# Kernel optimization log

Hardware: AMD Instinct MI355X
Metric: run time of the kernel (lower is better)

Reference implementation:

```python
import jax, jax.numpy as jnp
import numpy as np

N_X = 250_000
N_SRC = 50_000
N_Y = 50_000
N_INT = 500_000
E_NODE = 1_000_000
E_DOM = 500_000
H = 128
BN_EPS = 1e-5


def setup_inputs() -> dict:
    key = jax.random.key(0)
    ks = jax.random.split(key, 10)
    x = jax.random.normal(ks[0], (N_X, H), dtype=jnp.float32)
    y = jax.random.normal(ks[1], (N_Y, H), dtype=jnp.float32)
    domain_indicator = jnp.sort(jax.random.randint(ks[2], (N_X,), 0, N_SRC))
    node_map_edge_index = jax.random.randint(ks[3], (2, E_NODE), 0, N_X)
    intersect_indicator = jnp.sort(jax.random.randint(ks[4], (E_NODE,), 0, N_INT))
    domain_map_edge_index = jax.random.randint(ks[5], (2, E_DOM), 0, N_SRC)  # both rows < 50000 == N_SRC == N_Y
    W_xsum = jax.random.normal(ks[6], (H, H), dtype=jnp.float32) / np.sqrt(H)
    W_xint = jax.random.normal(ks[7], (H, H), dtype=jnp.float32) / np.sqrt(H)
    W_y = jax.random.normal(ks[8], (H, H), dtype=jnp.float32) / np.sqrt(H)
    bn_w = jnp.ones((H,), dtype=jnp.float32)
    bn_b = jnp.zeros((H,), dtype=jnp.float32)
    return {"x": x, "y": y, "domain_indicator": domain_indicator,
            "node_map_edge_index": node_map_edge_index,
            "intersect_indicator": intersect_indicator,
            "domain_map_edge_index": domain_map_edge_index,
            "W_xsum": W_xsum, "W_xint": W_xint, "W_y": W_y,
            "bn_w": bn_w, "bn_b": bn_b}


def reference(x, y, domain_indicator, node_map_edge_index, intersect_indicator,
              domain_map_edge_index, W_xsum, W_xint, W_y, bn_w, bn_b):
    # scatter_sum(x, source.domain_indicator) -> [N_SRC, H], then Linear (no bias)
    x_sum = jax.ops.segment_sum(x, domain_indicator, num_segments=N_SRC) @ W_xsum.T
    # gather nodes along node_map edges, scatter_sum into intersections -> [N_INT, H]
    x_int = jax.ops.segment_sum(x[node_map_edge_index[0]], intersect_indicator,
                                num_segments=N_INT) @ W_xint.T
    # per domain-map-edge messages, [E_DOM, H]
    x_msg = x_sum[domain_map_edge_index[0]] + x_int
    y_msg = y[domain_map_edge_index[1]] @ W_y.T
    msg = x_msg + y_msg
    # BatchNorm1d (training mode: batch stats, biased variance) + ReLU
    mean = jnp.mean(msg, axis=0)
    var = jnp.var(msg, axis=0)
    msg = (msg - mean) * jax.lax.rsqrt(var + BN_EPS) * bn_w + bn_b
    msg = jax.nn.relu(msg)
    # reduce messages onto target domains -> [N_Y, H]
    return jax.ops.segment_sum(msg, domain_map_edge_index[1], num_segments=N_Y)
```

## Files before the change

### kernel.cpp

```cpp
#include <hip/hip_runtime.h>
#include <cstdint>

#define HH 128
#define SB 136
constexpr int cN_X   = 250000;
constexpr int cN_SRC = 50000;
constexpr int cN_Y   = 50000;
constexpr int cN_INT = 500000;
constexpr int cE_NODE = 1000000;
constexpr int cE_DOM  = 500000;

typedef __attribute__((ext_vector_type(8))) short bf16x8;
typedef __attribute__((ext_vector_type(4))) float f32x4;

__device__ __forceinline__ float bf2f(unsigned short s) {
  union { unsigned u; float f; } v; v.u = ((unsigned)s) << 16; return v.f;
}
__device__ __forceinline__ unsigned short f2bf(float f) {
  union { float f; unsigned u; } v; v.f = f;
  unsigned r = v.u + 0x7fffu + ((v.u >> 16) & 1u);
  return (unsigned short)(r >> 16);
}

__global__ __launch_bounds__(256) void k_setup(const float* __restrict__ w0,
                                               const float* __restrict__ w1,
                                               const float* __restrict__ w2,
                                               unsigned short* __restrict__ dst,
                                               const int* __restrict__ ii,
                                               int* __restrict__ bnd,
                                               float* __restrict__ xsum,
                                               int* __restrict__ cnt,
                                               float* __restrict__ part2) {
  int b = blockIdx.x, tid = threadIdx.x;
  if (b < 48) {
    int i = b * 256 + tid;
    int idx4 = i * 4;
    int mat = idx4 >> 14;
    int off = idx4 & 16383;
    const float* src = (mat == 0) ? w0 : (mat == 1) ? w1 : w2;
    float4 v = *(const float4*)(src + off);
    ushort4 u;
    u.x = f2bf(v.x); u.y = f2bf(v.y); u.z = f2bf(v.z); u.w = f2bf(v.w);
    *(ushort4*)(dst + (size_t)mat * 16384 + off) = u;
    return;
  }
  b -= 48;
  if (b < 6250) {
    ((float4*)xsum)[(size_t)b * 256 + tid] = make_float4(0.f, 0.f, 0.f, 0.f);
    return;
  }
  b -= 6250;
  if (b < 49) {
    int i = b * 256 + tid;
    if (i < 12500) ((int4*)cnt)[i] = make_int4(0, 0, 0, 0);
    return;
  }
  b -= 49;
  if (b < 16) {
    ((float4*)part2)[b * 256 + tid] = make_float4(0.f, 0.f, 0.f, 0.f);
    return;
  }
  b -= 16;
  {
    int j = b * 256 + tid;
    if (j > cE_NODE) return;
    if (j == cE_NODE) {
      int a = ii[cE_NODE - 1];
      for (int e = a + 1; e <= cN_INT; ++e) bnd[e] = cE_NODE;
      return;
    }
    int bb = ii[j];
    int a = (j == 0) ? -1 : ii[j - 1];
    for (int e = a + 1; e <= bb; ++e) bnd[e] = j;
  }
}

__device__ __forceinline__ void load_bfrags(const unsigned short* __restrict__ Wbf,
                                            int wv, int lane, bf16x8 bfrag[2][4]) {
  int cbase = wv * 32 + (lane & 15);
  int krow = (lane >> 4) * 8;
#pragma unroll
  for (int ct = 0; ct < 2; ct++)
#pragma unroll
    for (int kt = 0; kt < 4; kt++)
      bfrag[ct][kt] = *(const bf16x8*)(Wbf + (size_t)(cbase + ct * 16) * HH + kt * 32 + krow);
}

__global__ __launch_bounds__(256, 4) void k_gemmx_segsum(
    const float* __restrict__ A, const int* __restrict__ ind,
    const unsigned short* __restrict__ Wbf,
    unsigned short* __restrict__ outb, float* __restrict__ xsum,
    const int* __restrict__ dme1, int* __restrict__ cnt) {
  __shared__ unsigned short sA[64 * SB];
  __shared__ int sind[64];
  int tid = threadIdx.x, lane = tid & 63, wv = tid >> 6;
  {
    int e = blockIdx.x * 256 + tid;
    if (e < cE_DOM) atomicAdd(&cnt[dme1[e]], 1);
  }
  int row0 = blockIdx.x * 64;
  int rows = min(64, cN_X - row0);
  if (tid < 64 && tid < rows) sind[tid] = ind[row0 + tid];
  bf16x8 bfrag[2][4];
  load_bfrags(Wbf, wv, lane, bfrag);
#pragma unroll
  for (int it = 0; it < 4; it++) {
    int g = it * 2048 + tid * 8;
    int r = g >> 7, c = g & 127;
    bf16x8 v = {0, 0, 0, 0, 0, 0, 0, 0};
    if (r < rows) {
      float4 f0 = *(const float4*)(A + (size_t)(row0 + r) * HH + c);
      float4 f1 = *(const float4*)(A + (size_t)(row0 + r) * HH + c + 4);
      v[0] = (short)f2bf(f0.x); v[1] = (short)f2bf(f0.y);
      v[2] = (short)f2bf(f0.z); v[3] = (short)f2bf(f0.w);
      v[4] = (short)f2bf(f1.x); v[5] = (short)f2bf(f1.y);
      v[6] = (short)f2bf(f1.z); v[7] = (short)f2bf(f1.w);
    }
    *(bf16x8*)(&sA[r * SB + c]) = v;
  }
  __syncthreads();
  {
    int rbase = wv * 16;
    if (rbase < rows) {
      int nr = min(16, rows - rbase);
      int c0 = lane * 2;
      unsigned xv[16];
#pragma unroll
      for (int k = 0; k < 16; k++)
        xv[k] = (k < nr) ? *(const unsigned*)(&sA[(rbase + k) * SB + c0]) : 0u;
      float a0 = 0.f, a1 = 0.f;
      int cur = sind[rbase];
      bool inside = false;
#pragma unroll
      for (int k = 0; k < 16; k++) {
        if (k < nr) {
          int s = sind[rbase + k];
          if (s != cur) {
            if (inside) {
              xsum[(size_t)cur * HH + c0] = a0;
              xsum[(size_t)cur * HH + c0 + 1] = a1;
            } else {
              atomicAdd(&xsum[(size_t)cur * HH + c0], a0);
              atomicAdd(&xsum[(size_t)cur * HH + c0 + 1], a1);
            }
            cur = s; a0 = 0.f; a1 = 0.f; inside = true;
          }
          a0 += bf2f(xv[k] & 0xffff); a1 += bf2f(xv[k] >> 16);
        }
      }
      atomicAdd(&xsum[(size_t)cur * HH + c0], a0);
      atomicAdd(&xsum[(size_t)cur * HH + c0 + 1], a1);
    }
  }
  int m = lane & 15, q = lane >> 4;
  f32x4 acc[4][2];
#pragma unroll
  for (int rt = 0; rt < 4; rt++)
#pragma unroll
    for (int ct = 0; ct < 2; ct++) acc[rt][ct] = (f32x4){0.f, 0.f, 0.f, 0.f};
#pragma unroll
  for (int kt = 0; kt < 4; kt++) {
    int kof = kt * 32 + q * 8;
#pragma unroll
    for (int rt = 0; rt < 4; rt++) {
      bf16x8 af = *(const bf16x8*)(&sA[(rt * 16 + m) * SB + kof]);
      acc[rt][0] = __builtin_amdgcn_mfma_f32_16x16x32_bf16(af, bfrag[0][kt], acc[rt][0], 0, 0, 0);
      acc[rt][1] = __builtin_amdgcn_mfma_f32_16x16x32_bf16(af, bfrag[1][kt], acc[rt][1], 0, 0, 0);
    }
  }
  __syncthreads();
  unsigned short* sC = sA;
#pragma unroll
  for (int rt = 0; rt < 4; rt++)
#pragma unroll
    for (int ct = 0; ct < 2; ct++)
#pragma unroll
      for (int rg = 0; rg < 4; rg++) {
        int r = rt * 16 + q * 4 + rg;
        sC[r * HH + wv * 32 + ct * 16 + m] = f2bf(acc[rt][ct][rg]);
      }
  __syncthreads();
  for (int i = tid; i < rows * 16; i += 256) {
    int r = i >> 4, g = i & 15;
    ((uint4*)(outb + (size_t)(row0 + r) * HH))[g] = ((const uint4*)(sC + r * HH))[g];
  }
}

__global__ __launch_bounds__(256, 4) void k_gemm2(const float* __restrict__ Axs,
                                                  const float* __restrict__ Ay,
                                                  const unsigned short* __restrict__ Wbf,
                                                  unsigned short* __restrict__ xsl,
                                                  unsigned short* __restrict__ ylin) {
  __shared__ unsigned short sA[64 * SB];
  int tid = threadIdx.x, lane = tid & 63, wv = tid >> 6;
  const int nbm = (cN_SRC + 63) / 64;
  bool isY = blockIdx.x >= nbm;
  const float* A = isY ? Ay : Axs;
  const unsigned short* W = Wbf + (isY ? 16384 : 0);
  unsigned short* outb = isY ? ylin : xsl;
  int bb = isY ? blockIdx.x - nbm : blockIdx.x;
  int row0 = bb * 64;
  int rows = min(64, cN_SRC - row0);
  bf16x8 bfrag[2][4];
  load_bfrags(W, wv, lane, bfrag);
#pragma unroll
  for (int it = 0; it < 4; it++) {
    int g = it * 2048 + tid * 8;
    int r = g >> 7, c = g & 127;
    bf16x8 v = {0, 0, 0, 0, 0, 0, 0, 0};
    if (r < rows) {
      float4 f0 = *(const float4*)(A + (size_t)(row0 + r) * HH + c);
      float4 f1 = *(const float4*)(A + (size_t)(row0 + r) * HH + c + 4);
      v[0] = (short)f2bf(f0.x); v[1] = (short)f2bf(f0.y);
      v[2] = (short)f2bf(f0.z); v[3] = (short)f2bf(f0.w);
      v[4] = (short)f2bf(f1.x); v[5] = (short)f2bf(f1.y);
      v[6] = (short)f2bf(f1.z); v[7] = (short)f2bf(f1.w);
    }
    *(bf16x8*)(&sA[r * SB + c]) = v;
  }
  __syncthreads();
  int m = lane & 15, q = lane >> 4;
  f32x4 acc[4][2];
#pragma unroll
  for (int rt = 0; rt < 4; rt++)
#pragma unroll
    for (int ct = 0; ct < 2; ct++) acc[rt][ct] = (f32x4){0.f, 0.f, 0.f, 0.f};
#pragma unroll
  for (int kt = 0; kt < 4; kt++) {
    int kof = kt * 32 + q * 8;
#pragma unroll
    for (int rt = 0; rt < 4; rt++) {
      bf16x8 af = *(const bf16x8*)(&sA[(rt * 16 + m) * SB + kof]);
      acc[rt][0] = __builtin_amdgcn_mfma_f32_16x16x32_bf16(af, bfrag[0][kt], acc[rt][0], 0, 0, 0);
      acc[rt][1] = __builtin_amdgcn_mfma_f32_16x16x32_bf16(af, bfrag[1][kt], acc[rt][1], 0, 0, 0);
    }
  }
  __syncthreads();
  unsigned short* sC = sA;
#pragma unroll
  for (int rt = 0; rt < 4; rt++)
#pragma unroll
    for (int ct = 0; ct < 2; ct++)
#pragma unroll
      for (int rg = 0; rg < 4; rg++) {
        int r = rt * 16 + q * 4 + rg;
        sC[r * HH + wv * 32 + ct * 16 + m] = f2bf(acc[rt][ct][rg]);
      }
  __syncthreads();
  for (int i = tid; i < rows * 16; i += 256) {
    int r = i >> 4, g = i & 15;
    ((uint4*)(outb + (size_t)(row0 + r) * HH))[g] = ((const uint4*)(sC + r * HH))[g];
  }
}

__global__ __launch_bounds__(256) void k_scan1(const int* __restrict__ cnt,
                                               int* __restrict__ bsum, int* __restrict__ excl) {
  __shared__ int buf[256];
  int i = blockIdx.x * 256 + threadIdx.x;
  int v = (i < cN_SRC) ? cnt[i] : 0;
  buf[threadIdx.x] = v; __syncthreads();
  for (int d = 1; d < 256; d <<= 1) {
    int t = (threadIdx.x >= d) ? buf[threadIdx.x - d] : 0;
    __syncthreads();
    buf[threadIdx.x] += t;
    __syncthreads();
  }
  if (i < cN_SRC) excl[i] = buf[threadIdx.x] - v;
  if (threadIdx.x == 255) bsum[blockIdx.x] = buf[255];
}
__global__ __launch_bounds__(256) void k_scan23(const int* __restrict__ excl,
                                                const int* __restrict__ bsum,
                                                int* __restrict__ offs,
                                                int* __restrict__ cursor, int nb) {
  __shared__ int buf[256];
  __shared__ int ex[256];
  int tid = threadIdx.x;
  int v = (tid < nb) ? bsum[tid] : 0;
  buf[tid] = v; __syncthreads();
  for (int d = 1; d < 256; d <<= 1) {
    int t = (tid >= d) ? buf[tid - d] : 0;
    __syncthreads();
    buf[tid] += t;
    __syncthreads();
  }
  ex[tid] = buf[tid] - v;
  __syncthreads();
  int i = blockIdx.x * 256 + tid;
  if (i < cN_SRC) { int o = excl[i] + ex[i >> 8]; offs[i] = o; cursor[i] = o; }
  else if (i == cN_SRC) offs[cN_SRC] = cE_DOM;
}
__global__ void k_scatter(const int* __restrict__ dme0, const int* __restrict__ dme1,
                          const int* __restrict__ bnd, int* __restrict__ cursor,
                          int4* __restrict__ rec) {
  int e = blockIdx.x * blockDim.x + threadIdx.x;
  if (e < cE_DOM) {
    int t = dme1[e];
    int pos = atomicAdd(&cursor[t], 1);
    int j0 = bnd[e];
    rec[pos] = make_int4(dme0[e], t, j0, bnd[e + 1] - j0);
  }
}

#define EDGE_ISSUE(I, B)                                                     \
  do {                                                                       \
    int le_ = wv * 8 + (I);                                                  \
    int n_ = __builtin_amdgcn_readfirstlane(sR[le_].w);                      \
    _Pragma("unroll")                                                        \
    for (int k_ = 0; k_ < 4; k_++) {                                         \
      int r_ = (k_ < n_) ? __builtin_amdgcn_readlane(idxv[I], k_) : 0;       \
      ub[B][k_] = xwu[(size_t)r_ * 64 + lane];                               \
    }                                                                        \
  } while (0)

#define EDGE_CONSUME(I, B)                                                   \
  do {                                                                       \
    int le_ = wv * 8 + (I);                                                  \
    int j0_ = __builtin_amdgcn_readfirstlane(sR[le_].z);                     \
    int n_ = __builtin_amdgcn_readfirstlane(sR[le_].w);                      \
    float a0_ = 0.f, a1_ = 0.f;                                              \
    _Pragma("unroll")                                                        \
    for (int k_ = 0; k_ < 4; k_++) {                                         \
      unsigned uv_ = (k_ < n_) ? ub[B][k_] : 0u;                             \
      a0_ += bf2f(uv_ & 0xffff);                                             \
      a1_ += bf2f(uv_ >> 16);                                                \
    }                                                                        \
    if (n_ > 4) {                                                            \
      for (int k_ = 4; k_ < n_; k_++) {                                      \
        int r_ = (k_ < 64) ? __builtin_amdgcn_readlane(idxv[I], k_)          \
                           : nme0[j0_ + k_];                                 \
        unsigned uu_ = xwu[(size_t)r_ * 64 + lane];                          \
        a0_ += bf2f(uu_ & 0xffff);                                           \
        a1_ += bf2f(uu_ >> 16);                                              \
      }                                                                      \
    }                                                                        \
    float m0_ = a0_ + bf2f(xs[I] & 0xffff) + bf2f(yy[I] & 0xffff);           \
    float m1_ = a1_ + bf2f(xs[I] >> 16) + bf2f(yy[I] >> 16);                 \
    unsigned um_ = ((unsigned)f2bf(m1_) << 16) | (unsigned)f2bf(m0_);        \
    __builtin_nontemporal_store(um_, &msgu[(size_t)(e0 + le_) * 64 + lane]); \
    s0 += m0_; q0 += m0_ * m0_; s1 += m1_; q1 += m1_ * m1_;                  \
  } while (0)

#define SBAR __builtin_amdgcn_sched_barrier(0)

__global__ __launch_bounds__(256, 8) void k_edge2(
    const unsigned* __restrict__ xwu, const int* __restrict__ nme0,
    const unsigned* __restrict__ xslu, const unsigned* __restrict__ ylu,
    const int4* __restrict__ rec,
    unsigned* __restrict__ msgu, float* __restrict__ part2) {
  __shared__ int4 sR[32];
  __shared__ float sBN[1024];
  int tid = threadIdx.x, lane = tid & 63, wv = tid >> 6;
  int e0 = blockIdx.x * 32;
  if (tid < 32) sR[tid] = rec[e0 + tid];
  __syncthreads();

  unsigned xs[8], yy[8];
  int idxv[8];
#pragma unroll
  for (int i = 0; i < 8; i++) {
    int le = wv * 8 + i;
    int s  = __builtin_amdgcn_readfirstlane(sR[le].x);
    int t  = __builtin_amdgcn_readfirstlane(sR[le].y);
    int j0 = __builtin_amdgcn_readfirstlane(sR[le].z);
    int n  = __builtin_amdgcn_readfirstlane(sR[le].w);
    xs[i] = xslu[(size_t)s * 64 + lane];
    yy[i] = ylu[(size_t)t * 64 + lane];
    idxv[i] = (lane < n) ? nme0[j0 + lane] : 0;
  }
  SBAR;

  float s0 = 0.f, q0 = 0.f, s1 = 0.f, q1 = 0.f;
  unsigned ub[3][4];
  EDGE_ISSUE(0, 0); SBAR;
  EDGE_ISSUE(1, 1); SBAR;
  EDGE_ISSUE(2, 2); SBAR;
  EDGE_CONSUME(0, 0);
  EDGE_ISSUE(3, 0); SBAR;
  EDGE_CONSUME(1, 1);
  EDGE_ISSUE(4, 1); SBAR;
  EDGE_CONSUME(2, 2);
  EDGE_ISSUE(5, 2); SBAR;
  EDGE_CONSUME(3, 0);
  EDGE_ISSUE(6, 0); SBAR;
  EDGE_CONSUME(4, 1);
  EDGE_ISSUE(7, 1); SBAR;
  EDGE_CONSUME(5, 2);
  EDGE_CONSUME(6, 0);
  EDGE_CONSUME(7, 1);

  *(float4*)(&sBN[wv * 256 + lane * 4]) = make_float4(s0, q0, s1, q1);
  __syncthreads();
  float v = sBN[tid] + sBN[256 + tid] + sBN[512 + tid] + sBN[768 + tid];
  atomicAdd(&part2[((blockIdx.x & 63) << 8) + tid], v);
}

__global__ __launch_bounds__(256) void k_bnfinal(const float* __restrict__ part2,
                                                 const float* __restrict__ bnw,
                                                 const float* __restrict__ bnb,
                                                 float* __restrict__ ss) {
  __shared__ float L[256];
  float s = 0.f;
  for (int b = 0; b < 64; b++) s += part2[b * 256 + threadIdx.x];
  L[threadIdx.x] = s; __syncthreads();
  if (threadIdx.x < HH) {
    int c = threadIdx.x;
    float sum = L[2 * c], sq = L[2 * c + 1];
    float mean = sum / (float)cE_DOM;
    float var = sq / (float)cE_DOM - mean * mean;
    float sc = bnw[c] * rsqrtf(var + 1e-5f);
    float sh = bnb[c] - mean * sc;
    ss[2 * c] = sc; ss[2 * c + 1] = sh;
  }
}

__global__ __launch_bounds__(256, 8) void k_out2(const unsigned* __restrict__ msgu,
                                                 const int* __restrict__ offs,
                                                 const float* __restrict__ ss,
                                                 float* __restrict__ out) {
  int wv = threadIdx.x >> 6, lane = threadIdx.x & 63;
  int t = blockIdx.x * 4 + wv;
  if (t >= cN_Y) return;
  int c0 = lane * 2;
  float sc0 = ss[c0 * 2 + 0], sh0 = ss[c0 * 2 + 1];
  float sc1 = ss[c0 * 2 + 2], sh1 = ss[c0 * 2 + 3];
  int j0 = __builtin_amdgcn_readfirstlane(offs[t]);
  int j1 = __builtin_amdgcn_readfirstlane(offs[t + 1]);
  float a0 = 0.f, a1 = 0.f;
  int p = j0;
  for (; p + 8 <= j1; p += 8) {
    unsigned m[8];
#pragma unroll
    for (int k = 0; k < 8; k++) m[k] = msgu[(size_t)(p + k) * 64 + lane];
    __builtin_amdgcn_sched_barrier(0);
#pragma unroll
    for (int k = 0; k < 8; k++) {
      a0 += fmaxf(fmaf(bf2f(m[k] & 0xffff), sc0, sh0), 0.f);
      a1 += fmaxf(fmaf(bf2f(m[k] >> 16), sc1, sh1), 0.f);
    }
  }
  if (p + 4 <= j1) {
    unsigned m[4];
#pragma unroll
    for (int k = 0; k < 4; k++) m[k] = msgu[(size_t)(p + k) * 64 + lane];
    __builtin_amdgcn_sched_barrier(0);
#pragma unroll
    for (int k = 0; k < 4; k++) {
      a0 += fmaxf(fmaf(bf2f(m[k] & 0xffff), sc0, sh0), 0.f);
      a1 += fmaxf(fmaf(bf2f(m[k] >> 16), sc1, sh1), 0.f);
    }
    p += 4;
  }
  for (; p < j1; p++) {
    unsigned m = msgu[(size_t)p * 64 + lane];
    a0 += fmaxf(fmaf(bf2f(m & 0xffff), sc0, sh0), 0.f);
    a1 += fmaxf(fmaf(bf2f(m >> 16), sc1, sh1), 0.f);
  }
  *(float2*)(out + (size_t)t * HH + c0) = make_float2(a0, a1);
}

extern "C" void kernel_launch(void* const* d_in, const int* in_sizes, int n_in,
                              void* d_out, int out_size, void* d_ws, size_t ws_size,
                              hipStream_t stream) {
  const float* x     = (const float*)d_in[0];
  const float* y     = (const float*)d_in[1];
  const int* dom_ind = (const int*)d_in[2];
  const int* nme     = (const int*)d_in[3];
  const int* ii      = (const int*)d_in[4];
  const int* dme     = (const int*)d_in[5];
  const float* Wxsum = (const float*)d_in[6];
  const float* Wxint = (const float*)d_in[7];
  const float* Wy    = (const float*)d_in[8];
  const float* bnw   = (const float*)d_in[9];
  const float* bnb   = (const float*)d_in[10];
  float* out = (float*)d_out;

  char* ws = (char*)d_ws;
  size_t o = 0;
  auto alloc = [&](size_t bytes) -> void* {
    void* p = ws + o;
    o = (o + bytes + 255) & ~(size_t)255;
    return p;
  };
  float* xsum   = (float*)alloc((size_t)cN_SRC * HH * 4);
  unsigned short* xsl = (unsigned short*)alloc((size_t)cN_SRC * HH * 2);
  unsigned short* ylin = (unsigned short*)alloc((size_t)cN_Y * HH * 2);
  unsigned short* xw = (unsigned short*)alloc((size_t)cN_X * HH * 2);
  unsigned short* msg = (unsigned short*)alloc((size_t)cE_DOM * HH * 2);
  int* bnd      = (int*)alloc((size_t)(cN_INT + 1) * 4);
  int* cnt      = (int*)alloc((size_t)cN_SRC * 4);
  int* excl     = (int*)alloc((size_t)cN_SRC * 4);
  int* bsum     = (int*)alloc(256 * 4);
  int* offs     = (int*)alloc((size_t)(cN_SRC + 1) * 4);
  int* cursor   = (int*)alloc((size_t)cN_SRC * 4);
  int4* rec     = (int4*)alloc((size_t)cE_DOM * 16);
  float* part2  = (float*)alloc(64 * 256 * 4);
  float* ssbuf  = (float*)alloc(256 * 4);
  unsigned short* Wbf = (unsigned short*)alloc(3 * 16384 * 2);

  const int nb_scan = (cN_SRC + 255) / 256;
  k_setup<<<48 + 6250 + 49 + 16 + 3907, 256, 0, stream>>>(Wxsum, Wy, Wxint, Wbf,
                                                          ii, bnd, xsum, cnt, part2);
  k_gemmx_segsum<<<(cN_X + 63) / 64, 256, 0, stream>>>(x, dom_ind, Wbf + 32768, xw, xsum,
                                                       dme + cE_DOM, cnt);
  k_gemm2<<<2 * ((cN_SRC + 63) / 64), 256, 0, stream>>>(xsum, y, Wbf, xsl, ylin);
  k_scan1<<<nb_scan, 256, 0, stream>>>(cnt, bsum, excl);
  k_scan23<<<(cN_SRC + 1 + 255) / 256, 256, 0, stream>>>(excl, bsum, offs, cursor, nb_scan);
  k_scatter<<<(cE_DOM + 255) / 256, 256, 0, stream>>>(dme, dme + cE_DOM, bnd, cursor, rec);
  k_edge2<<<cE_DOM / 32, 256, 0, stream>>>((const unsigned*)xw, nme,
                                           (const unsigned*)xsl, (const unsigned*)ylin,
                                           rec, (unsigned*)msg, part2);
  k_bnfinal<<<1, 256, 0, stream>>>(part2, bnw, bnb, ssbuf);
  k_out2<<<(cN_Y + 3) / 4, 256, 0, stream>>>((const unsigned*)msg, offs, ssbuf, out);
}
```

Baseline: 425.7 us.

## Fold y GEMM into setup, merge scan/scatter into cooperative kernel

The y@W_y GEMM moves into the setup kernel, since it depends only on inputs, and runs alongside the zeroing and boundary work. The separate weight-to-bf16 conversion is dropped, with each GEMM converting its fp32 weights directly into fragments. The two scan kernels and the scatter kernel become one cooperative kernel that uses grid syncs. This removes several launches and serial dependencies, at the cost of redundant weight conversion per block and the overhead of cooperative grid sync.

Measured after the change: 687.1 us. 61.4% more time.

```diff
diff --git a/kernel.cpp b/kernel.cpp
--- a/kernel.cpp
+++ b/kernel.cpp
@@ -1,5 +1,8 @@
 #include <hip/hip_runtime.h>
+#include <hip/hip_cooperative_groups.h>
 #include <cstdint>
+
+namespace cg = cooperative_groups;
 
 #define HH 128
 #define SB 136
@@ -22,29 +25,101 @@
   return (unsigned short)(r >> 16);
 }
 
-__global__ __launch_bounds__(256) void k_setup(const float* __restrict__ w0,
-                                               const float* __restrict__ w1,
-                                               const float* __restrict__ w2,
-                                               unsigned short* __restrict__ dst,
+__device__ __forceinline__ void load_bfrags_f32(const float* __restrict__ Wf,
+                                                int wv, int lane, bf16x8 bfrag[2][4]) {
+  int cbase = wv * 32 + (lane & 15);
+  int krow = (lane >> 4) * 8;
+#pragma unroll
+  for (int ct = 0; ct < 2; ct++)
+#pragma unroll
+    for (int kt = 0; kt < 4; kt++) {
+      const float* p = Wf + (size_t)(cbase + ct * 16) * HH + kt * 32 + krow;
+      float4 f0 = *(const float4*)p;
+      float4 f1 = *(const float4*)(p + 4);
+      bf16x8 v;
+      v[0] = (short)f2bf(f0.x); v[1] = (short)f2bf(f0.y);
+      v[2] = (short)f2bf(f0.z); v[3] = (short)f2bf(f0.w);
+      v[4] = (short)f2bf(f1.x); v[5] = (short)f2bf(f1.y);
+      v[6] = (short)f2bf(f1.z); v[7] = (short)f2bf(f1.w);
+      bfrag[ct][kt] = v;
+    }
+}
+
+__device__ __forceinline__ void gemm_tile(const float* __restrict__ A,
+                                          const float* __restrict__ Wf,
+                                          unsigned short* __restrict__ outb,
+                                          int row0, int rows,
+                                          unsigned short* sA, int tid) {
+  int lane = tid & 63, wv = tid >> 6;
+  bf16x8 bfrag[2][4];
+  load_bfrags_f32(Wf, wv, lane, bfrag);
+#pragma unroll
+  for (int it = 0; it < 4; it++) {
+    int g = it * 2048 + tid * 8;
+    int r = g >> 7, c = g & 127;
+    bf16x8 v = {0, 0, 0, 0, 0, 0, 0, 0};
+    if (r < rows) {
+      float4 f0 = *(const float4*)(A + (size_t)(row0 + r) * HH + c);
+      float4 f1 = *(const float4*)(A + (size_t)(row0 + r) * HH + c + 4);
+      v[0] = (short)f2bf(f0.x); v[1] = (short)f2bf(f0.y);
+      v[2] = (short)f2bf(f0.z); v[3] = (short)f2bf(f0.w);
+      v[4] = (short)f2bf(f1.x); v[5] = (short)f2bf(f1.y);
+      v[6] = (short)f2bf(f1.z); v[7] = (short)f2bf(f1.w);
+    }
+    *(bf16x8*)(&sA[r * SB + c]) = v;
+  }
+  __syncthreads();
+  int m = lane & 15, q = lane >> 4;
+  f32x4 acc[4][2];
+#pragma unroll
+  for (int rt = 0; rt < 4; rt++)
+#pragma unroll
+    for (int ct = 0; ct < 2; ct++) acc[rt][ct] = (f32x4){0.f, 0.f, 0.f, 0.f};
+#pragma unroll
+  for (int kt = 0; kt < 4; kt++) {
+    int kof = kt * 32 + q * 8;
+#pragma unroll
+    for (int rt = 0; rt < 4; rt++) {
+      bf16x8 af = *(const bf16x8*)(&sA[(rt * 16 + m) * SB + kof]);
+      acc[rt][0] = __builtin_amdgcn_mfma_f32_16x16x32_bf16(af, bfrag[0][kt], acc[rt][0], 0, 0, 0);
+      acc[rt][1] = __builtin_amdgcn_mfma_f32_16x16x32_bf16(af, bfrag[1][kt], acc[rt][1], 0, 0, 0);
+    }
+  }
+  __syncthreads();
+  unsigned short* sC = sA;
+#pragma unroll
+  for (int rt = 0; rt < 4; rt++)
+#pragma unroll
+    for (int ct = 0; ct < 2; ct++)
+#pragma unroll
+      for (int rg = 0; rg < 4; rg++) {
+        int r = rt * 16 + q * 4 + rg;
+        sC[r * HH + wv * 32 + ct * 16 + m] = f2bf(acc[rt][ct][rg]);
+      }
+  __syncthreads();
+  for (int i = tid; i < rows * 16; i += 256) {
+    int r = i >> 4, g = i & 15;
+    ((uint4*)(outb + (size_t)(row0 + r) * HH))[g] = ((const uint4*)(sC + r * HH))[g];
+  }
+}
+
+__global__ __launch_bounds__(256) void k_setup(const float* __restrict__ y,
+                                               const float* __restrict__ Wy,
+                                               unsigned short* __restrict__ ylin,
                                                const int* __restrict__ ii,
                                                int* __restrict__ bnd,
                                                float* __restrict__ xsum,
                                                int* __restrict__ cnt,
                                                float* __restrict__ part2) {
+  __shared__ unsigned short sA[64 * SB];
   int b = blockIdx.x, tid = threadIdx.x;
-  if (b < 48) {
-    int i = b * 256 + tid;
-    int idx4 = i * 4;
-    int mat = idx4 >> 14;
-    int off = idx4 & 16383;
-    const float* src = (mat == 0) ? w0 : (mat == 1) ? w1 : w2;
-    float4 v = *(const float4*)(src + off);
-    ushort4 u;
-    u.x = f2bf(v.x); u.y = f2bf(v.y); u.z = f2bf(v.z); u.w = f2bf(v.w);
-    *(ushort4*)(dst + (size_t)mat * 16384 + off) = u;
+  if (b < 782) {
+    int row0 = b * 64;
+    int rows = min(64, cN_Y - row0);
+    gemm_tile(y, Wy, ylin, row0, rows, sA, tid);
     return;
   }
-  b -= 48;
+  b -= 782;
   if (b < 6250) {
     ((float4*)xsum)[(size_t)b * 256 + tid] = make_float4(0.f, 0.f, 0.f, 0.f);
     return;
@@ -75,20 +150,9 @@
   }
 }
 
-__device__ __forceinline__ void load_bfrags(const unsigned short* __restrict__ Wbf,
-                                            int wv, int lane, bf16x8 bfrag[2][4]) {
-  int cbase = wv * 32 + (lane & 15);
-  int krow = (lane >> 4) * 8;
-#pragma unroll
-  for (int ct = 0; ct < 2; ct++)
-#pragma unroll
-    for (int kt = 0; kt < 4; kt++)
-      bfrag[ct][kt] = *(const bf16x8*)(Wbf + (size_t)(cbase + ct * 16) * HH + kt * 32 + krow);
-}
-
 __global__ __launch_bounds__(256, 4) void k_gemmx_segsum(
     const float* __restrict__ A, const int* __restrict__ ind,
-    const unsigned short* __restrict__ Wbf,
+    const float* __restrict__ Wxint,
     unsigned short* __restrict__ outb, float* __restrict__ xsum,
     const int* __restrict__ dme1, int* __restrict__ cnt) {
   __shared__ unsigned short sA[64 * SB];
@@ -102,7 +166,7 @@
   int rows = min(64, cN_X - row0);
   if (tid < 64 && tid < rows) sind[tid] = ind[row0 + tid];
   bf16x8 bfrag[2][4];
-  load_bfrags(Wbf, wv, lane, bfrag);
+  load_bfrags_f32(Wxint, wv, lane, bfrag);
 #pragma unroll
   for (int it = 0; it < 4; it++) {
     int g = it * 2048 + tid * 8;
@@ -186,114 +250,60 @@
   }
 }
 
-__global__ __launch_bounds__(256, 4) void k_gemm2(const float* __restrict__ Axs,
-                                                  const float* __restrict__ Ay,
-                                                  const unsigned short* __restrict__ Wbf,
-                                                  unsigned short* __restrict__ xsl,
-                                                  unsigned short* __restrict__ ylin) {
+__global__ __launch_bounds__(256, 4) void k_gemmxsl(const float* __restrict__ xsum,
+                                                    const float* __restrict__ Wxsum,
+                                                    unsigned short* __restrict__ xsl) {
   __shared__ unsigned short sA[64 * SB];
-  int tid = threadIdx.x, lane = tid & 63, wv = tid >> 6;
-  const int nbm = (cN_SRC + 63) / 64;
-  bool isY = blockIdx.x >= nbm;
-  const float* A = isY ? Ay : Axs;
-  const unsigned short* W = Wbf + (isY ? 16384 : 0);
-  unsigned short* outb = isY ? ylin : xsl;
-  int bb = isY ? blockIdx.x - nbm : blockIdx.x;
-  int row0 = bb * 64;
+  int row0 = blockIdx.x * 64;
   int rows = min(64, cN_SRC - row0);
-  bf16x8 bfrag[2][4];
-  load_bfrags(W, wv, lane, bfrag);
-#pragma unroll
-  for (int it = 0; it < 4; it++) {
-    int g = it * 2048 + tid * 8;
-    int r = g >> 7, c = g & 127;
-    bf16x8 v = {0, 0, 0, 0, 0, 0, 0, 0};
-    if (r < rows) {
-      float4 f0 = *(const float4*)(A + (size_t)(row0 + r) * HH + c);
-      float4 f1 = *(const float4*)(A + (size_t)(row0 + r) * HH + c + 4);
-      v[0] = (short)f2bf(f0.x); v[1] = (short)f2bf(f0.y);
-      v[2] = (short)f2bf(f0.z); v[3] = (short)f2bf(f0.w);
-      v[4] = (short)f2bf(f1.x); v[5] = (short)f2bf(f1.y);
-      v[6] = (short)f2bf(f1.z); v[7] = (short)f2bf(f1.w);
-    }
-    *(bf16x8*)(&sA[r * SB + c]) = v;
-  }
-  __syncthreads();
-  int m = lane & 15, q = lane >> 4;
-  f32x4 acc[4][2];
-#pragma unroll
-  for (int rt = 0; rt < 4; rt++)
-#pragma unroll
-    for (int ct = 0; ct < 2; ct++) acc[rt][ct] = (f32x4){0.f, 0.f, 0.f, 0.f};
-#pragma unroll
-  for (int kt = 0; kt < 4; kt++) {
-    int kof = kt * 32 + q * 8;
-#pragma unroll
-    for (int rt = 0; rt < 4; rt++) {
-      bf16x8 af = *(const bf16x8*)(&sA[(rt * 16 + m) * SB + kof]);
-      acc[rt][0] = __builtin_amdgcn_mfma_f32_16x16x32_bf16(af, bfrag[0][kt], acc[rt][0], 0, 0, 0);
-      acc[rt][1] = __builtin_amdgcn_mfma_f32_16x16x32_bf16(af, bfrag[1][kt], acc[rt][1], 0, 0, 0);
-    }
-  }
-  __syncthreads();
-  unsigned short* sC = sA;
-#pragma unroll
-  for (int rt = 0; rt < 4; rt++)
-#pragma unroll
-    for (int ct = 0; ct < 2; ct++)
-#pragma unroll
-      for (int rg = 0; rg < 4; rg++) {
-        int r = rt * 16 + q * 4 + rg;
-        sC[r * HH + wv * 32 + ct * 16 + m] = f2bf(acc[rt][ct][rg]);
-      }
-  __syncthreads();
-  for (int i = tid; i < rows * 16; i += 256) {
-    int r = i >> 4, g = i & 15;
-    ((uint4*)(outb + (size_t)(row0 + r) * HH))[g] = ((const uint4*)(sC + r * HH))[g];
-  }
-}
-
-__global__ __launch_bounds__(256) void k_scan1(const int* __restrict__ cnt,
-                                               int* __restrict__ bsum, int* __restrict__ excl) {
-  __shared__ int buf[256];
-  int i = blockIdx.x * 256 + threadIdx.x;
-  int v = (i < cN_SRC) ? cnt[i] : 0;
-  buf[threadIdx.x] = v; __syncthreads();
-  for (int d = 1; d < 256; d <<= 1) {
-    int t = (threadIdx.x >= d) ? buf[threadIdx.x - d] : 0;
-    __syncthreads();
-    buf[threadIdx.x] += t;
-    __syncthreads();
-  }
-  if (i < cN_SRC) excl[i] = buf[threadIdx.x] - v;
-  if (threadIdx.x == 255) bsum[blockIdx.x] = buf[255];
-}
-__global__ __launch_bounds__(256) void k_scan23(const int* __restrict__ excl,
-                                                const int* __restrict__ bsum,
+  gemm_tile(xsum, Wxsum, xsl, row0, rows, sA, threadIdx.x);
+}
+
+__global__ __launch_bounds__(256, 4) void k_csr(const int* __restrict__ cnt,
+                                                int* __restrict__ bsum,
+                                                int* __restrict__ excl,
                                                 int* __restrict__ offs,
-                                                int* __restrict__ cursor, int nb) {
+                                                int* __restrict__ cursor,
+                                                const int* __restrict__ dme0,
+                                                const int* __restrict__ dme1,
+                                                const int* __restrict__ bnd,
+                                                int4* __restrict__ rec) {
+  cg::grid_group grid = cg::this_grid();
   __shared__ int buf[256];
   __shared__ int ex[256];
+  const int nb = (cN_SRC + 255) / 256;
   int tid = threadIdx.x;
-  int v = (tid < nb) ? bsum[tid] : 0;
-  buf[tid] = v; __syncthreads();
-  for (int d = 1; d < 256; d <<= 1) {
-    int t = (tid >= d) ? buf[tid - d] : 0;
+  if (blockIdx.x < nb) {
+    int i = blockIdx.x * 256 + tid;
+    int v = (i < cN_SRC) ? cnt[i] : 0;
+    buf[tid] = v; __syncthreads();
+    for (int d = 1; d < 256; d <<= 1) {
+      int t = (tid >= d) ? buf[tid - d] : 0;
+      __syncthreads();
+      buf[tid] += t;
+      __syncthreads();
+    }
+    if (i < cN_SRC) excl[i] = buf[tid] - v;
+    if (tid == 255) bsum[blockIdx.x] = buf[255];
+  }
+  grid.sync();
+  {
+    int v = (tid < nb) ? bsum[tid] : 0;
+    buf[tid] = v; __syncthreads();
+    for (int d = 1; d < 256; d <<= 1) {
+      int t = (tid >= d) ? buf[tid - d] : 0;
+      __syncthreads();
+      buf[tid] += t;
+      __syncthreads();
+    }
+    ex[tid] = buf[tid] - v;
     __syncthreads();
-    buf[tid] += t;
-    __syncthreads();
-  }
-  ex[tid] = buf[tid] - v;
-  __syncthreads();
-  int i = blockIdx.x * 256 + tid;
-  if (i < cN_SRC) { int o = excl[i] + ex[i >> 8]; offs[i] = o; cursor[i] = o; }
-  else if (i == cN_SRC) offs[cN_SRC] = cE_DOM;
-}
-__global__ void k_scatter(const int* __restrict__ dme0, const int* __restrict__ dme1,
-                          const int* __restrict__ bnd, int* __restrict__ cursor,
-                          int4* __restrict__ rec) {
-  int e = blockIdx.x * blockDim.x + threadIdx.x;
-  if (e < cE_DOM) {
+    int i = blockIdx.x * 256 + tid;
+    if (i < cN_SRC) { int o = excl[i] + ex[i >> 8]; offs[i] = o; cursor[i] = o; }
+    else if (i == cN_SRC) offs[cN_SRC] = cE_DOM;
+  }
+  grid.sync();
+  for (int e = blockIdx.x * 256 + tid; e < cE_DOM; e += gridDim.x * 256) {
     int t = dme1[e];
     int pos = atomicAdd(&cursor[t], 1);
     int j0 = bnd[e];
@@ -495,17 +505,21 @@
   int4* rec     = (int4*)alloc((size_t)cE_DOM * 16);
   float* part2  = (float*)alloc(64 * 256 * 4);
   float* ssbuf  = (float*)alloc(256 * 4);
-  unsigned short* Wbf = (unsigned short*)alloc(3 * 16384 * 2);
-
-  const int nb_scan = (cN_SRC + 255) / 256;
-  k_setup<<<48 + 6250 + 49 + 16 + 3907, 256, 0, stream>>>(Wxsum, Wy, Wxint, Wbf,
-                                                          ii, bnd, xsum, cnt, part2);
-  k_gemmx_segsum<<<(cN_X + 63) / 64, 256, 0, stream>>>(x, dom_ind, Wbf + 32768, xw, xsum,
+
+  k_setup<<<782 + 6250 + 49 + 16 + 3907, 256, 0, stream>>>(y, Wy, ylin, ii, bnd,
+                                                           xsum, cnt, part2);
+  k_gemmx_segsum<<<(cN_X + 63) / 64, 256, 0, stream>>>(x, dom_ind, Wxint, xw, xsum,
                                                        dme + cE_DOM, cnt);
-  k_gemm2<<<2 * ((cN_SRC + 63) / 64), 256, 0, stream>>>(xsum, y, Wbf, xsl, ylin);
-  k_scan1<<<nb_scan, 256, 0, stream>>>(cnt, bsum, excl);
-  k_scan23<<<(cN_SRC + 1 + 255) / 256, 256, 0, stream>>>(excl, bsum, offs, cursor, nb_scan);
-  k_scatter<<<(cE_DOM + 255) / 256, 256, 0, stream>>>(dme, dme + cE_DOM, bnd, cursor, rec);
+  k_gemmxsl<<<(cN_SRC + 63) / 64, 256, 0, stream>>>(xsum, Wxsum, xsl);
+  {
+    const int* dme0p = dme;
+    const int* dme1p = dme + cE_DOM;
+    void* csrArgs[] = {(void*)&cnt, (void*)&bsum, (void*)&excl, (void*)&offs,
+                       (void*)&cursor, (void*)&dme0p, (void*)&dme1p,
+                       (void*)&bnd, (void*)&rec};
+    hipLaunchCooperativeKernel((const void*)k_csr, dim3(1024), dim3(256),
+                               csrArgs, 0, stream);
+  }
   k_edge2<<<cE_DOM / 32, 256, 0, stream>>>((const unsigned*)xw, nme,
                                            (const unsigned*)xsl, (const unsigned*)ylin,
                                            rec, (unsigned*)msg, part2);
```
